# Kernel tuning notes

Measured on AMD Instinct MI355X. Metric: run time of the kernel, lower is better.

The kernel has to match this reference:

```python
import jax, jax.numpy as jnp
import numpy as np

L, B, S, D, H, FF = 6, 4, 1024, 256, 8, 128
DH = D // H
EPS = 1e-5


def _ln(x, w, b):
    m = x.mean(-1, keepdims=True)
    v = ((x - m) ** 2).mean(-1, keepdims=True)
    return (x - m) / jnp.sqrt(v + EPS) * w + b


def setup_inputs() -> dict:
    key = jax.random.key(0)
    ks = jax.random.split(key, 6)
    s = lambda k, shape: jax.random.normal(k, shape, jnp.float32) * 0.02
    return {
        "x": jax.random.normal(ks[0], (B, S, D), jnp.float32),
        "ln1_w": jnp.ones((L, D), jnp.float32),
        "ln1_b": jnp.zeros((L, D), jnp.float32),
        "wqkv": s(ks[1], (L, D, 3 * D)),   # qkv_linear, bias=False
        "wout": s(ks[2], (L, D, D)),       # out_linear, bias=False
        "ln2_w": jnp.ones((L, D), jnp.float32),
        "ln2_b": jnp.zeros((L, D), jnp.float32),
        "w1": s(ks[3], (L, D, 2 * FF)),    # Linear(d_model, 2*ff)
        "b1": jnp.zeros((L, 2 * FF), jnp.float32),
        "w2": s(ks[4], (L, FF, D)),        # Linear(ff, d_model)
        "b2": jnp.zeros((L, D), jnp.float32),
    }


def reference(x, ln1_w, ln1_b, wqkv, wout, ln2_w, ln2_b, w1, b1, w2, b2):
    attn_weights_list = []
    scale = 1.0 / jnp.sqrt(jnp.float32(DH))
    for i in range(L):
        # --- pre-norm multi-head attention ---
        xn = _ln(x, ln1_w[i], ln1_b[i])
        qkv = xn @ wqkv[i]                       # [B,S,3D]
        q, k, v = jnp.split(qkv, 3, axis=-1)
        rs = lambda t: t.reshape(B, S, H, DH).transpose(0, 2, 1, 3)  # b h s d
        q, k, v = rs(q), rs(k), rs(v)
        logits = jnp.einsum('bhid,bhjd->bhij', q, k) * scale
        aw = jax.nn.softmax(logits, axis=-1)     # [B,H,S,S] (dropout=0, eval)
        attn_weights_list.append(aw)
        o = jnp.einsum('bhij,bhjd->bhid', aw, v)
        o = o.transpose(0, 2, 1, 3).reshape(B, S, D) @ wout[i]
        x = x + o
        # --- pre-norm GEGLU FFN ---
        h = _ln(x, ln2_w[i], ln2_b[i]) @ w1[i] + b1[i]   # [B,S,2*FF]
        a, g = jnp.split(h, 2, axis=-1)
        x = x + (a * jax.nn.gelu(g, approximate=False)) @ w2[i] + b2[i]
    return x, jnp.stack(attn_weights_list)      # [B,S,D], [L,B,H,S,S]
```

## Files before the change

### kernel.cpp

```cpp
#include <hip/hip_runtime.h>
#include <hip/hip_bf16.h>

typedef __bf16 bf16x8 __attribute__((ext_vector_type(8)));
typedef __bf16 bf16x4 __attribute__((ext_vector_type(4)));
typedef __bf16 bf16x2 __attribute__((ext_vector_type(2)));
typedef float  f32x4  __attribute__((ext_vector_type(4)));

#define LAYERS 6
#define BATCH  4
#define SEQ    1024
#define DMODEL 256
#define NHEAD  8
#define DHEAD  32
#define FFDIM  128
#define ROWS   (BATCH*SEQ)
#define QKVN   (3*DMODEL)
#define QSCALE 0.2550348616f

static __device__ __forceinline__ bf16x8 ldg8(const __bf16* p) {
  return *reinterpret_cast<const bf16x8*>(p);
}
#define MFMA16(a, b, c) __builtin_amdgcn_mfma_f32_16x16x32_bf16((a), (b), (c), 0, 0, 0)

__global__ void k_prep(const float* __restrict__ wqkv, const float* __restrict__ wout,
                       const float* __restrict__ w1, const float* __restrict__ w2,
                       __bf16* __restrict__ wqkvT, __bf16* __restrict__ woutT,
                       __bf16* __restrict__ w1T, __bf16* __restrict__ w2T) {
  const int N1 = LAYERS * DMODEL * QKVN;
  const int N2 = LAYERS * DMODEL * DMODEL;
  const int N3 = LAYERS * DMODEL * 2 * FFDIM;
  const int N4 = LAYERS * FFDIM * DMODEL;
  int total = N1 + N2 + N3 + N4;
  for (int i = blockIdx.x * blockDim.x + threadIdx.x; i < total; i += gridDim.x * blockDim.x) {
    int j = i;
    if (j < N1) {
      int l = j / (DMODEL * QKVN), rc = j - l * (DMODEL * QKVN);
      int r = rc / QKVN, c = rc - r * QKVN;
      wqkvT[(size_t)l * DMODEL * QKVN + (size_t)c * DMODEL + r] = (__bf16)wqkv[j]; continue;
    } j -= N1;
    if (j < N2) {
      int l = j / (DMODEL * DMODEL), rc = j - l * (DMODEL * DMODEL);
      int r = rc / DMODEL, c = rc - r * DMODEL;
      woutT[(size_t)l * DMODEL * DMODEL + (size_t)c * DMODEL + r] = (__bf16)wout[j]; continue;
    } j -= N2;
    if (j < N3) {
      int l = j / (DMODEL * 2 * FFDIM), rc = j - l * (DMODEL * 2 * FFDIM);
      int r = rc / (2 * FFDIM), c = rc - r * (2 * FFDIM);
      w1T[(size_t)l * DMODEL * 2 * FFDIM + (size_t)c * DMODEL + r] = (__bf16)w1[j]; continue;
    } j -= N3;
    {
      int l = j / (FFDIM * DMODEL), rc = j - l * (FFDIM * DMODEL);
      int r = rc / DMODEL, c = rc - r * DMODEL;
      w2T[(size_t)l * FFDIM * DMODEL + (size_t)c * FFDIM + r] = (__bf16)w2[j];
    }
  }
}

__global__ __launch_bounds__(64) void k_ln(const float* __restrict__ x,
                                           const float* __restrict__ w,
                                           const float* __restrict__ b,
                                           __bf16* __restrict__ out) {
  int row = blockIdx.x, l = threadIdx.x;
  const float* xr = x + (size_t)row * DMODEL;
  float v[4];
  #pragma unroll
  for (int j = 0; j < 4; ++j) v[j] = xr[l + 64 * j];
  float s = v[0] + v[1] + v[2] + v[3];
  #pragma unroll
  for (int off = 32; off >= 1; off >>= 1) s += __shfl_xor(s, off);
  float mean = s * (1.0f / DMODEL);
  float sq = 0.f;
  #pragma unroll
  for (int j = 0; j < 4; ++j) { v[j] -= mean; sq += v[j] * v[j]; }
  #pragma unroll
  for (int off = 32; off >= 1; off >>= 1) sq += __shfl_xor(sq, off);
  float rstd = rsqrtf(sq * (1.0f / DMODEL) + 1e-5f);
  __bf16* orow = out + (size_t)row * DMODEL;
  #pragma unroll
  for (int j = 0; j < 4; ++j) {
    int c = l + 64 * j;
    orow[c] = (__bf16)(v[j] * rstd * w[c] + b[c]);
  }
}

__global__ __launch_bounds__(256) void k_qkv(const __bf16* __restrict__ xn,
                                             const __bf16* __restrict__ Bt,
                                             __bf16* __restrict__ qb,
                                             __bf16* __restrict__ kt,
                                             __bf16* __restrict__ vt) {
  int w = threadIdx.x >> 6, l = threadIdx.x & 63, lr = l & 15, lg = l >> 4;
  int m0 = blockIdx.x * 64 + w * 16;
  int n0 = blockIdx.y * 64;
  f32x4 acc[4] = {};
  const __bf16* ap = xn + (size_t)(m0 + lr) * DMODEL + 8 * lg;
  const __bf16* bp = Bt + (size_t)(n0 + lr) * DMODEL + 8 * lg;
  for (int kc = 0; kc < DMODEL; kc += 32) {
    bf16x8 a = ldg8(ap + kc);
    #pragma unroll
    for (int t = 0; t < 4; ++t) {
      bf16x8 b = ldg8(bp + (size_t)t * 16 * DMODEL + kc);
      acc[t] = MFMA16(a, b, acc[t]);
    }
  }
  int row = m0 + lg * 4;
  if (n0 < DMODEL) {
    #pragma unroll
    for (int t = 0; t < 4; ++t) {
      int col = n0 + t * 16 + lr;
      #pragma unroll
      for (int r = 0; r < 4; ++r)
        qb[(size_t)(row + r) * DMODEL + col] = (__bf16)(acc[t][r] * QSCALE);
    }
  } else if (n0 < 2 * DMODEL) {
    int b_ = row >> 10, s = row & (SEQ - 1);
    #pragma unroll
    for (int t = 0; t < 4; ++t) {
      int hdh = n0 - DMODEL + t * 16 + lr;
      int h = hdh >> 5, dh = hdh & 31;
      size_t base = ((size_t)(b_ * NHEAD + h) * SEQ + s) * DHEAD + dh;
      #pragma unroll
      for (int r = 0; r < 4; ++r) kt[base + (size_t)r * DHEAD] = (__bf16)acc[t][r];
    }
  } else {
    int b_ = row >> 10, s = row & (SEQ - 1);
    #pragma unroll
    for (int t = 0; t < 4; ++t) {
      int hdh = n0 - 2 * DMODEL + t * 16 + lr;
      int h = hdh >> 5, dh = hdh & 31;
      bf16x4 v4;
      #pragma unroll
      for (int r = 0; r < 4; ++r) v4[r] = (__bf16)acc[t][r];
      *reinterpret_cast<bf16x4*>(vt + ((size_t)(b_ * NHEAD + h) * DHEAD + dh) * SEQ + s) = v4;
    }
  }
}

__global__ __launch_bounds__(512, 6) void k_attn(const __bf16* __restrict__ qb,
                                                 const __bf16* __restrict__ kt,
                                                 const __bf16* __restrict__ vt,
                                                 __bf16* __restrict__ ob,
                                                 float* __restrict__ aw) {
  __shared__ __bf16 P[8][2][16][40];
  __shared__ float  Ssum[8][16];
  __shared__ float  OS[8][16][34];
  int bid = blockIdx.x;
  int swz = (bid & 7) * 256 + (bid >> 3);
  int qblk = swz & 63, h = (swz >> 6) & 7, b = swz >> 9;
  int w = threadIdx.x >> 6, l = threadIdx.x & 63, lr = l & 15, lg = l >> 4;
  int q0 = qblk * 16;
  bf16x8 qf = ldg8(qb + ((size_t)(b * SEQ) + q0 + lr) * DMODEL + h * DHEAD + 8 * lg);
  const __bf16* ktb = kt + (size_t)(b * NHEAD + h) * SEQ * DHEAD + 8 * lg;
  const __bf16* vtb = vt + (size_t)(b * NHEAD + h) * DHEAD * SEQ;
  f32x4 z = {};
  int kbeg = w * 128;

  float s4[4] = {0.f, 0.f, 0.f, 0.f};
  #pragma unroll 4
  for (int t = 0; t < 8; ++t) {
    bf16x8 kf = ldg8(ktb + (size_t)(kbeg + t * 16 + lr) * DHEAD);
    f32x4 d = MFMA16(qf, kf, z);
    #pragma unroll
    for (int r = 0; r < 4; ++r) s4[r] += exp2f(d[r]);
  }
  #pragma unroll
  for (int off = 1; off < 16; off <<= 1) {
    #pragma unroll
    for (int r = 0; r < 4; ++r) s4[r] += __shfl_xor(s4[r], off);
  }
  if (lr == 0) {
    #pragma unroll
    for (int r = 0; r < 4; ++r) Ssum[w][lg * 4 + r] = s4[r];
  }
  __syncthreads();
  float rinv[4];
  #pragma unroll
  for (int r = 0; r < 4; ++r) {
    int row = lg * 4 + r;
    float s = Ssum[0][row] + Ssum[1][row] + Ssum[2][row] + Ssum[3][row]
            + Ssum[4][row] + Ssum[5][row] + Ssum[6][row] + Ssum[7][row];
    rinv[r] = 1.0f / s;
  }

  float* awb = aw + ((size_t)(b * NHEAD + h) * SEQ) * SEQ;

#define QK_TILE(KC, BUF)                                                          \
  {                                                                               \
    _Pragma("unroll")                                                             \
    for (int half = 0; half < 2; ++half) {                                        \
      int k0 = (KC) + half * 16;                                                  \
      bf16x8 kf = ldg8(ktb + (size_t)(k0 + lr) * DHEAD);                          \
      f32x4 d = MFMA16(qf, kf, z);                                                \
      _Pragma("unroll")                                                           \
      for (int r = 0; r < 4; ++r) {                                               \
        float pv = exp2f(d[r]);                                                   \
        __builtin_nontemporal_store(pv * rinv[r],                                 \
            &awb[(size_t)(q0 + lg * 4 + r) * SEQ + k0 + lr]);                     \
        P[w][BUF][lg * 4 + r][half * 16 + lr] = (__bf16)pv;                       \
      }                                                                           \
    }                                                                             \
  }

  f32x4 accO[2] = {};
  QK_TILE(kbeg, 0)
  #pragma unroll
  for (int j = 1; j < 4; ++j) {
    int kc = kbeg + j * 32;
    bf16x8 pf  = *reinterpret_cast<const bf16x8*>(&P[w][(j - 1) & 1][lr][8 * lg]);
    bf16x8 vf0 = ldg8(vtb + (size_t)lr * SEQ + (kc - 32) + 8 * lg);
    bf16x8 vf1 = ldg8(vtb + (size_t)(16 + lr) * SEQ + (kc - 32) + 8 * lg);
    QK_TILE(kc, j & 1)
    accO[0] = MFMA16(pf, vf0, accO[0]);
    accO[1] = MFMA16(pf, vf1, accO[1]);
  }
  {
    bf16x8 pf  = *reinterpret_cast<const bf16x8*>(&P[w][1][lr][8 * lg]);
    bf16x8 vf0 = ldg8(vtb + (size_t)lr * SEQ + (kbeg + 96) + 8 * lg);
    bf16x8 vf1 = ldg8(vtb + (size_t)(16 + lr) * SEQ + (kbeg + 96) + 8 * lg);
    accO[0] = MFMA16(pf, vf0, accO[0]);
    accO[1] = MFMA16(pf, vf1, accO[1]);
  }
#undef QK_TILE

  #pragma unroll
  for (int t = 0; t < 2; ++t)
    #pragma unroll
    for (int r = 0; r < 4; ++r) OS[w][lg * 4 + r][t * 16 + lr] = accO[t][r] * rinv[r];
  __syncthreads();
  int row = threadIdx.x >> 5, col = threadIdx.x & 31;
  float o = 0.f;
  #pragma unroll
  for (int ww = 0; ww < 8; ++ww) o += OS[ww][row][col];
  ob[((size_t)(b * SEQ) + q0 + row) * DMODEL + h * DHEAD + col] = (__bf16)o;
}

template <int LAST>
__global__ __launch_bounds__(512) void k_pf(const __bf16* __restrict__ ob,
                                            const __bf16* __restrict__ woutT,
                                            const float* __restrict__ xres,
                                            const float* __restrict__ ln2w,
                                            const float* __restrict__ ln2b,
                                            const __bf16* __restrict__ w1t,
                                            const float* __restrict__ b1,
                                            const __bf16* __restrict__ w2t,
                                            const float* __restrict__ b2,
                                            float* __restrict__ x32out,
                                            const float* __restrict__ lnw_n,
                                            const float* __restrict__ lnb_n,
                                            const __bf16* __restrict__ wqkvT_n,
                                            __bf16* __restrict__ qb,
                                            __bf16* __restrict__ kt,
                                            __bf16* __restrict__ vt,
                                            float* __restrict__ xout) {
  __shared__ float  xs[16][268];
  __shared__ __bf16 XN[16][264];
  __shared__ __bf16 G[16][136];
  __shared__ __bf16 HT[16][136];
  int w = threadIdx.x >> 6, l = threadIdx.x & 63, lr = l & 15, lg = l >> 4;
  int m0 = blockIdx.x * 16;
  {
    int n0 = w * 32;
    f32x4 acc[2] = {};
    const __bf16* ap = ob + (size_t)(m0 + lr) * DMODEL + 8 * lg;
    const __bf16* bp = woutT + (size_t)(n0 + lr) * DMODEL + 8 * lg;
    for (int kc = 0; kc < DMODEL; kc += 32) {
      bf16x8 a = ldg8(ap + kc);
      #pragma unroll
      for (int t = 0; t < 2; ++t)
        acc[t] = MFMA16(a, ldg8(bp + (size_t)t * 16 * DMODEL + kc), acc[t]);
    }
    #pragma unroll
    for (int t = 0; t < 2; ++t) {
      int col = n0 + t * 16 + lr;
      #pragma unroll
      for (int r = 0; r < 4; ++r) {
        int row = lg * 4 + r;
        xs[row][col] = acc[t][r] + xres[(size_t)(m0 + row) * DMODEL + col];
      }
    }
  }
  __syncthreads();
  #pragma unroll
  for (int rr = 0; rr < 2; ++rr) {
    int row = w * 2 + rr;
    f32x4 v = *reinterpret_cast<const f32x4*>(&xs[row][4 * l]);
    float s = v[0] + v[1] + v[2] + v[3];
    #pragma unroll
    for (int off = 32; off >= 1; off >>= 1) s += __shfl_xor(s, off);
    float mean = s * (1.0f / DMODEL);
    float sq = 0.f;
    f32x4 c;
    #pragma unroll
    for (int j = 0; j < 4; ++j) { c[j] = v[j] - mean; sq += c[j] * c[j]; }
    #pragma unroll
    for (int off = 32; off >= 1; off >>= 1) sq += __shfl_xor(sq, off);
    float rstd = rsqrtf(sq * (1.0f / DMODEL) + 1e-5f);
    f32x4 lwv = *reinterpret_cast<const f32x4*>(&ln2w[4 * l]);
    f32x4 lbv = *reinterpret_cast<const f32x4*>(&ln2b[4 * l]);
    bf16x4 o4;
    #pragma unroll
    for (int j = 0; j < 4; ++j) o4[j] = (__bf16)(c[j] * rstd * lwv[j] + lbv[j]);
    *reinterpret_cast<bf16x4*>(&XN[row][4 * l]) = o4;
  }
  __syncthreads();
  int n0f = w * 32;
  f32x4 acc1[2] = {};
  {
    const __bf16* bp = w1t + (size_t)(n0f + lr) * DMODEL + 8 * lg;
    for (int kc = 0; kc < DMODEL; kc += 32) {
      bf16x8 a = *reinterpret_cast<const bf16x8*>(&XN[lr][kc + 8 * lg]);
      #pragma unroll
      for (int t = 0; t < 2; ++t)
        acc1[t] = MFMA16(a, ldg8(bp + (size_t)t * 16 * DMODEL + kc), acc1[t]);
    }
  }
  if (w >= 4) {
    #pragma unroll
    for (int t = 0; t < 2; ++t) {
      int col = n0f + t * 16 + lr;
      #pragma unroll
      for (int r = 0; r < 4; ++r) {
        float g = acc1[t][r] + b1[col];
        float ge = 0.5f * g * (1.0f + erff(g * 0.70710678118654752f));
        G[lg * 4 + r][col - 128] = (__bf16)ge;
      }
    }
  }
  __syncthreads();
  if (w < 4) {
    #pragma unroll
    for (int t = 0; t < 2; ++t) {
      int col = n0f + t * 16 + lr;
      #pragma unroll
      for (int r = 0; r < 4; ++r) {
        float a1 = acc1[t][r] + b1[col];
        HT[lg * 4 + r][col] = (__bf16)(a1 * (float)G[lg * 4 + r][col]);
      }
    }
  }
  __syncthreads();
  {
    f32x4 acc2[2] = {};
    const __bf16* bp = w2t + (size_t)(n0f + lr) * FFDIM + 8 * lg;
    for (int kc = 0; kc < FFDIM; kc += 32) {
      bf16x8 a2 = *reinterpret_cast<const bf16x8*>(&HT[lr][kc + 8 * lg]);
      #pragma unroll
      for (int t = 0; t < 2; ++t)
        acc2[t] = MFMA16(a2, ldg8(bp + (size_t)t * 16 * FFDIM + kc), acc2[t]);
    }
    #pragma unroll
    for (int t = 0; t < 2; ++t) {
      int col = n0f + t * 16 + lr;
      #pragma unroll
      for (int r = 0; r < 4; ++r) {
        int row = lg * 4 + r;
        xs[row][col] = acc2[t][r] + b2[col] + xs[row][col];
      }
    }
  }
  __syncthreads();
  #pragma unroll
  for (int rr = 0; rr < 2; ++rr) {
    int row = w * 2 + rr;
    f32x4 v = *reinterpret_cast<const f32x4*>(&xs[row][4 * l]);
    if (LAST) {
      *reinterpret_cast<f32x4*>(&xout[(size_t)(m0 + row) * DMODEL + 4 * l]) = v;
    } else {
      float s = v[0] + v[1] + v[2] + v[3];
      #pragma unroll
      for (int off = 32; off >= 1; off >>= 1) s += __shfl_xor(s, off);
      float mean = s * (1.0f / DMODEL);
      float sq = 0.f;
      f32x4 c;
      #pragma unroll
      for (int j = 0; j < 4; ++j) { c[j] = v[j] - mean; sq += c[j] * c[j]; }
      #pragma unroll
      for (int off = 32; off >= 1; off >>= 1) sq += __shfl_xor(sq, off);
      float rstd = rsqrtf(sq * (1.0f / DMODEL) + 1e-5f);
      *reinterpret_cast<f32x4*>(&x32out[(size_t)(m0 + row) * DMODEL + 4 * l]) = v;
      f32x4 lwv = *reinterpret_cast<const f32x4*>(&lnw_n[4 * l]);
      f32x4 lbv = *reinterpret_cast<const f32x4*>(&lnb_n[4 * l]);
      bf16x4 o4;
      #pragma unroll
      for (int j = 0; j < 4; ++j) o4[j] = (__bf16)(c[j] * rstd * lwv[j] + lbv[j]);
      *reinterpret_cast<bf16x4*>(&XN[row][4 * l]) = o4;
    }
  }
  if (!LAST) {
    __syncthreads();
    f32x4 acc[6] = {};
    {
      const __bf16* bp = wqkvT_n + (size_t)(w * 96 + lr) * DMODEL + 8 * lg;
      for (int kc = 0; kc < DMODEL; kc += 32) {
        bf16x8 a = *reinterpret_cast<const bf16x8*>(&XN[lr][kc + 8 * lg]);
        #pragma unroll
        for (int t = 0; t < 6; ++t)
          acc[t] = MFMA16(a, ldg8(bp + (size_t)t * 16 * DMODEL + kc), acc[t]);
      }
    }
    int row = m0 + lg * 4;
    int b_ = row >> 10, s = row & (SEQ - 1);
    #pragma unroll
    for (int t = 0; t < 6; ++t) {
      int col = w * 96 + t * 16 + lr;
      if (col < DMODEL) {
        #pragma unroll
        for (int r = 0; r < 4; ++r)
          qb[(size_t)(row + r) * DMODEL + col] = (__bf16)(acc[t][r] * QSCALE);
      } else if (col < 2 * DMODEL) {
        int hdh = col - DMODEL;
        int h = hdh >> 5, dh = hdh & 31;
        size_t base = ((size_t)(b_ * NHEAD + h) * SEQ + s) * DHEAD + dh;
        #pragma unroll
        for (int r = 0; r < 4; ++r) kt[base + (size_t)r * DHEAD] = (__bf16)acc[t][r];
      } else {
        int hdh = col - 2 * DMODEL;
        int h = hdh >> 5, dh = hdh & 31;
        bf16x4 v4;
        #pragma unroll
        for (int r = 0; r < 4; ++r) v4[r] = (__bf16)acc[t][r];
        *reinterpret_cast<bf16x4*>(vt + ((size_t)(b_ * NHEAD + h) * DHEAD + dh) * SEQ + s) = v4;
      }
    }
  }
}

static inline size_t align256(size_t x) { return (x + 255) & ~(size_t)255; }

extern "C" void kernel_launch(void* const* d_in, const int* in_sizes, int n_in,
                              void* d_out, int out_size, void* d_ws, size_t ws_size,
                              hipStream_t stream) {
  const float* x_in = (const float*)d_in[0];
  const float* ln1w = (const float*)d_in[1];
  const float* ln1b = (const float*)d_in[2];
  const float* wqkv = (const float*)d_in[3];
  const float* wout = (const float*)d_in[4];
  const float* ln2w = (const float*)d_in[5];
  const float* ln2b = (const float*)d_in[6];
  const float* w1   = (const float*)d_in[7];
  const float* b1   = (const float*)d_in[8];
  const float* w2   = (const float*)d_in[9];
  const float* b2   = (const float*)d_in[10];
  float* out = (float*)d_out;

  char* p = (char*)d_ws;
  float*  x32   = (float*)p;  p += align256((size_t)ROWS * DMODEL * 4);
  __bf16* xn    = (__bf16*)p; p += align256((size_t)ROWS * DMODEL * 2);
  __bf16* qb    = (__bf16*)p; p += align256((size_t)ROWS * DMODEL * 2);
  __bf16* kt    = (__bf16*)p; p += align256((size_t)ROWS * DMODEL * 2);
  __bf16* vt    = (__bf16*)p; p += align256((size_t)ROWS * DMODEL * 2);
  __bf16* ob    = (__bf16*)p; p += align256((size_t)ROWS * DMODEL * 2);
  __bf16* wqkvT = (__bf16*)p; p += align256((size_t)LAYERS * DMODEL * QKVN * 2);
  __bf16* woutT = (__bf16*)p; p += align256((size_t)LAYERS * DMODEL * DMODEL * 2);
  __bf16* w1T   = (__bf16*)p; p += align256((size_t)LAYERS * DMODEL * 2 * FFDIM * 2);
  __bf16* w2T   = (__bf16*)p; p += align256((size_t)LAYERS * FFDIM * DMODEL * 2);

  k_prep<<<2048, 256, 0, stream>>>(wqkv, wout, w1, w2, wqkvT, woutT, w1T, w2T);
  k_ln<<<ROWS, 64, 0, stream>>>(x_in, ln1w, ln1b, xn);
  k_qkv<<<dim3(ROWS / 64, QKVN / 64), 256, 0, stream>>>(xn, wqkvT, qb, kt, vt);

  const size_t AW_LAYER = (size_t)BATCH * NHEAD * SEQ * SEQ;
  for (int i = 0; i < LAYERS; ++i) {
    float* aw_l = out + (size_t)ROWS * DMODEL + (size_t)i * AW_LAYER;
    k_attn<<<SEQ / 16 * NHEAD * BATCH, 512, 0, stream>>>(qb, kt, vt, ob, aw_l);
    const float* xres = (i == 0) ? x_in : x32;
    if (i < LAYERS - 1) {
      k_pf<0><<<ROWS / 16, 512, 0, stream>>>(
          ob, woutT + (size_t)i * DMODEL * DMODEL, xres,
          ln2w + i * DMODEL, ln2b + i * DMODEL,
          w1T + (size_t)i * DMODEL * 2 * FFDIM, b1 + i * 2 * FFDIM,
          w2T + (size_t)i * FFDIM * DMODEL, b2 + i * DMODEL,
          x32, ln1w + (i + 1) * DMODEL, ln1b + (i + 1) * DMODEL,
          wqkvT + (size_t)(i + 1) * DMODEL * QKVN, qb, kt, vt, nullptr);
    } else {
      k_pf<1><<<ROWS / 16, 512, 0, stream>>>(
          ob, woutT + (size_t)i * DMODEL * DMODEL, xres,
          ln2w + i * DMODEL, ln2b + i * DMODEL,
          w1T + (size_t)i * DMODEL * 2 * FFDIM, b1 + i * 2 * FFDIM,
          w2T + (size_t)i * FFDIM * DMODEL, b2 + i * DMODEL,
          x32, nullptr, nullptr, nullptr, nullptr, nullptr, nullptr, out);
    }
  }
}
```

Baseline: 458.3 us.

## Fuse attention into post-attention FFN kernel with ping-pong QKV buffers

Merges the attention kernel and the out-projection/FFN/next-QKV kernel into one per-16-row block kernel. Each of the 8 waves now handles one head over the full sequence instead of splitting keys across waves, so the attention output stays in shared memory and the cross-wave reductions are no longer needed. QKV buffers are double-buffered because the next layer's Q/K/V are written while other blocks still read the current ones. This removes a launch and the global round trip of the attention output per layer. In exchange each wave runs a much longer serial key loop, grid parallelism per block drops, and larger shared memory may reduce occupancy.

```diff
diff --git a/kernel.cpp b/kernel.cpp
--- a/kernel.cpp
+++ b/kernel.cpp
@@ -3,7 +3,6 @@
 
 typedef __bf16 bf16x8 __attribute__((ext_vector_type(8)));
 typedef __bf16 bf16x4 __attribute__((ext_vector_type(4)));
-typedef __bf16 bf16x2 __attribute__((ext_vector_type(2)));
 typedef float  f32x4  __attribute__((ext_vector_type(4)));
 
 #define LAYERS 6
@@ -135,29 +134,46 @@
   }
 }
 
-__global__ __launch_bounds__(512, 6) void k_attn(const __bf16* __restrict__ qb,
-                                                 const __bf16* __restrict__ kt,
-                                                 const __bf16* __restrict__ vt,
-                                                 __bf16* __restrict__ ob,
-                                                 float* __restrict__ aw) {
+template <int LAST>
+__global__ __launch_bounds__(512) void k_mega(const __bf16* __restrict__ qb,
+                                              const __bf16* __restrict__ kt,
+                                              const __bf16* __restrict__ vt,
+                                              const __bf16* __restrict__ woutT,
+                                              const float* __restrict__ xres,
+                                              const float* __restrict__ ln2w,
+                                              const float* __restrict__ ln2b,
+                                              const __bf16* __restrict__ w1t,
+                                              const float* __restrict__ b1,
+                                              const __bf16* __restrict__ w2t,
+                                              const float* __restrict__ b2,
+                                              float* __restrict__ x32out,
+                                              const float* __restrict__ lnw_n,
+                                              const float* __restrict__ lnb_n,
+                                              const __bf16* __restrict__ wqkvT_n,
+                                              __bf16* __restrict__ qb_n,
+                                              __bf16* __restrict__ kt_n,
+                                              __bf16* __restrict__ vt_n,
+                                              float* __restrict__ aw,
+                                              float* __restrict__ xout) {
   __shared__ __bf16 P[8][2][16][40];
-  __shared__ float  Ssum[8][16];
-  __shared__ float  OS[8][16][34];
-  int bid = blockIdx.x;
-  int swz = (bid & 7) * 256 + (bid >> 3);
-  int qblk = swz & 63, h = (swz >> 6) & 7, b = swz >> 9;
+  __shared__ __bf16 OB[16][264];
+  __shared__ float  xs[16][268];
+  __shared__ __bf16 XN[16][264];
+  __shared__ __bf16 G[16][136];
+  __shared__ __bf16 HT[16][136];
   int w = threadIdx.x >> 6, l = threadIdx.x & 63, lr = l & 15, lg = l >> 4;
-  int q0 = qblk * 16;
-  bf16x8 qf = ldg8(qb + ((size_t)(b * SEQ) + q0 + lr) * DMODEL + h * DHEAD + 8 * lg);
-  const __bf16* ktb = kt + (size_t)(b * NHEAD + h) * SEQ * DHEAD + 8 * lg;
-  const __bf16* vtb = vt + (size_t)(b * NHEAD + h) * DHEAD * SEQ;
+  int m0 = blockIdx.x * 16;
+  int b = m0 >> 10, q0 = m0 & (SEQ - 1);
+
+  bf16x8 qf = ldg8(qb + (size_t)(m0 + lr) * DMODEL + w * DHEAD + 8 * lg);
+  const __bf16* ktb = kt + (size_t)(b * NHEAD + w) * SEQ * DHEAD + 8 * lg;
+  const __bf16* vtb = vt + (size_t)(b * NHEAD + w) * DHEAD * SEQ;
   f32x4 z = {};
-  int kbeg = w * 128;
 
   float s4[4] = {0.f, 0.f, 0.f, 0.f};
   #pragma unroll 4
-  for (int t = 0; t < 8; ++t) {
-    bf16x8 kf = ldg8(ktb + (size_t)(kbeg + t * 16 + lr) * DHEAD);
+  for (int t = 0; t < SEQ / 16; ++t) {
+    bf16x8 kf = ldg8(ktb + (size_t)(t * 16 + lr) * DHEAD);
     f32x4 d = MFMA16(qf, kf, z);
     #pragma unroll
     for (int r = 0; r < 4; ++r) s4[r] += exp2f(d[r]);
@@ -167,21 +183,11 @@
     #pragma unroll
     for (int r = 0; r < 4; ++r) s4[r] += __shfl_xor(s4[r], off);
   }
-  if (lr == 0) {
-    #pragma unroll
-    for (int r = 0; r < 4; ++r) Ssum[w][lg * 4 + r] = s4[r];
-  }
-  __syncthreads();
   float rinv[4];
   #pragma unroll
-  for (int r = 0; r < 4; ++r) {
-    int row = lg * 4 + r;
-    float s = Ssum[0][row] + Ssum[1][row] + Ssum[2][row] + Ssum[3][row]
-            + Ssum[4][row] + Ssum[5][row] + Ssum[6][row] + Ssum[7][row];
-    rinv[r] = 1.0f / s;
-  }
-
-  float* awb = aw + ((size_t)(b * NHEAD + h) * SEQ) * SEQ;
+  for (int r = 0; r < 4; ++r) rinv[r] = 1.0f / s4[r];
+
+  float* awb = aw + ((size_t)(b * NHEAD + w) * SEQ) * SEQ;
 
 #define QK_TILE(KC, BUF)                                                          \
   {                                                                               \
@@ -201,10 +207,10 @@
   }
 
   f32x4 accO[2] = {};
-  QK_TILE(kbeg, 0)
-  #pragma unroll
-  for (int j = 1; j < 4; ++j) {
-    int kc = kbeg + j * 32;
+  QK_TILE(0, 0)
+  #pragma unroll 2
+  for (int j = 1; j < SEQ / 32; ++j) {
+    int kc = j * 32;
     bf16x8 pf  = *reinterpret_cast<const bf16x8*>(&P[w][(j - 1) & 1][lr][8 * lg]);
     bf16x8 vf0 = ldg8(vtb + (size_t)lr * SEQ + (kc - 32) + 8 * lg);
     bf16x8 vf1 = ldg8(vtb + (size_t)(16 + lr) * SEQ + (kc - 32) + 8 * lg);
@@ -214,8 +220,8 @@
   }
   {
     bf16x8 pf  = *reinterpret_cast<const bf16x8*>(&P[w][1][lr][8 * lg]);
-    bf16x8 vf0 = ldg8(vtb + (size_t)lr * SEQ + (kbeg + 96) + 8 * lg);
-    bf16x8 vf1 = ldg8(vtb + (size_t)(16 + lr) * SEQ + (kbeg + 96) + 8 * lg);
+    bf16x8 vf0 = ldg8(vtb + (size_t)lr * SEQ + (SEQ - 32) + 8 * lg);
+    bf16x8 vf1 = ldg8(vtb + (size_t)(16 + lr) * SEQ + (SEQ - 32) + 8 * lg);
     accO[0] = MFMA16(pf, vf0, accO[0]);
     accO[1] = MFMA16(pf, vf1, accO[1]);
   }
@@ -224,46 +230,16 @@
   #pragma unroll
   for (int t = 0; t < 2; ++t)
     #pragma unroll
-    for (int r = 0; r < 4; ++r) OS[w][lg * 4 + r][t * 16 + lr] = accO[t][r] * rinv[r];
-  __syncthreads();
-  int row = threadIdx.x >> 5, col = threadIdx.x & 31;
-  float o = 0.f;
-  #pragma unroll
-  for (int ww = 0; ww < 8; ++ww) o += OS[ww][row][col];
-  ob[((size_t)(b * SEQ) + q0 + row) * DMODEL + h * DHEAD + col] = (__bf16)o;
-}
-
-template <int LAST>
-__global__ __launch_bounds__(512) void k_pf(const __bf16* __restrict__ ob,
-                                            const __bf16* __restrict__ woutT,
-                                            const float* __restrict__ xres,
-                                            const float* __restrict__ ln2w,
-                                            const float* __restrict__ ln2b,
-                                            const __bf16* __restrict__ w1t,
-                                            const float* __restrict__ b1,
-                                            const __bf16* __restrict__ w2t,
-                                            const float* __restrict__ b2,
-                                            float* __restrict__ x32out,
-                                            const float* __restrict__ lnw_n,
-                                            const float* __restrict__ lnb_n,
-                                            const __bf16* __restrict__ wqkvT_n,
-                                            __bf16* __restrict__ qb,
-                                            __bf16* __restrict__ kt,
-                                            __bf16* __restrict__ vt,
-                                            float* __restrict__ xout) {
-  __shared__ float  xs[16][268];
-  __shared__ __bf16 XN[16][264];
-  __shared__ __bf16 G[16][136];
-  __shared__ __bf16 HT[16][136];
-  int w = threadIdx.x >> 6, l = threadIdx.x & 63, lr = l & 15, lg = l >> 4;
-  int m0 = blockIdx.x * 16;
+    for (int r = 0; r < 4; ++r)
+      OB[lg * 4 + r][w * DHEAD + t * 16 + lr] = (__bf16)(accO[t][r] * rinv[r]);
+  __syncthreads();
+
   {
     int n0 = w * 32;
     f32x4 acc[2] = {};
-    const __bf16* ap = ob + (size_t)(m0 + lr) * DMODEL + 8 * lg;
     const __bf16* bp = woutT + (size_t)(n0 + lr) * DMODEL + 8 * lg;
     for (int kc = 0; kc < DMODEL; kc += 32) {
-      bf16x8 a = ldg8(ap + kc);
+      bf16x8 a = *reinterpret_cast<const bf16x8*>(&OB[lr][kc + 8 * lg]);
       #pragma unroll
       for (int t = 0; t < 2; ++t)
         acc[t] = MFMA16(a, ldg8(bp + (size_t)t * 16 * DMODEL + kc), acc[t]);
@@ -405,20 +381,20 @@
       if (col < DMODEL) {
         #pragma unroll
         for (int r = 0; r < 4; ++r)
-          qb[(size_t)(row + r) * DMODEL + col] = (__bf16)(acc[t][r] * QSCALE);
+          qb_n[(size_t)(row + r) * DMODEL + col] = (__bf16)(acc[t][r] * QSCALE);
       } else if (col < 2 * DMODEL) {
         int hdh = col - DMODEL;
         int h = hdh >> 5, dh = hdh & 31;
         size_t base = ((size_t)(b_ * NHEAD + h) * SEQ + s) * DHEAD + dh;
         #pragma unroll
-        for (int r = 0; r < 4; ++r) kt[base + (size_t)r * DHEAD] = (__bf16)acc[t][r];
+        for (int r = 0; r < 4; ++r) kt_n[base + (size_t)r * DHEAD] = (__bf16)acc[t][r];
       } else {
         int hdh = col - 2 * DMODEL;
         int h = hdh >> 5, dh = hdh & 31;
         bf16x4 v4;
         #pragma unroll
         for (int r = 0; r < 4; ++r) v4[r] = (__bf16)acc[t][r];
-        *reinterpret_cast<bf16x4*>(vt + ((size_t)(b_ * NHEAD + h) * DHEAD + dh) * SEQ + s) = v4;
+        *reinterpret_cast<bf16x4*>(vt_n + ((size_t)(b_ * NHEAD + h) * DHEAD + dh) * SEQ + s) = v4;
       }
     }
   }
@@ -445,10 +421,12 @@
   char* p = (char*)d_ws;
   float*  x32   = (float*)p;  p += align256((size_t)ROWS * DMODEL * 4);
   __bf16* xn    = (__bf16*)p; p += align256((size_t)ROWS * DMODEL * 2);
-  __bf16* qb    = (__bf16*)p; p += align256((size_t)ROWS * DMODEL * 2);
-  __bf16* kt    = (__bf16*)p; p += align256((size_t)ROWS * DMODEL * 2);
-  __bf16* vt    = (__bf16*)p; p += align256((size_t)ROWS * DMODEL * 2);
-  __bf16* ob    = (__bf16*)p; p += align256((size_t)ROWS * DMODEL * 2);
+  __bf16* qbA   = (__bf16*)p; p += align256((size_t)ROWS * DMODEL * 2);
+  __bf16* ktA   = (__bf16*)p; p += align256((size_t)ROWS * DMODEL * 2);
+  __bf16* vtA   = (__bf16*)p; p += align256((size_t)ROWS * DMODEL * 2);
+  __bf16* qbB   = (__bf16*)p; p += align256((size_t)ROWS * DMODEL * 2);
+  __bf16* ktB   = (__bf16*)p; p += align256((size_t)ROWS * DMODEL * 2);
+  __bf16* vtB   = (__bf16*)p; p += align256((size_t)ROWS * DMODEL * 2);
   __bf16* wqkvT = (__bf16*)p; p += align256((size_t)LAYERS * DMODEL * QKVN * 2);
   __bf16* woutT = (__bf16*)p; p += align256((size_t)LAYERS * DMODEL * DMODEL * 2);
   __bf16* w1T   = (__bf16*)p; p += align256((size_t)LAYERS * DMODEL * 2 * FFDIM * 2);
@@ -456,28 +434,35 @@
 
   k_prep<<<2048, 256, 0, stream>>>(wqkv, wout, w1, w2, wqkvT, woutT, w1T, w2T);
   k_ln<<<ROWS, 64, 0, stream>>>(x_in, ln1w, ln1b, xn);
-  k_qkv<<<dim3(ROWS / 64, QKVN / 64), 256, 0, stream>>>(xn, wqkvT, qb, kt, vt);
+  k_qkv<<<dim3(ROWS / 64, QKVN / 64), 256, 0, stream>>>(xn, wqkvT, qbA, ktA, vtA);
 
   const size_t AW_LAYER = (size_t)BATCH * NHEAD * SEQ * SEQ;
   for (int i = 0; i < LAYERS; ++i) {
     float* aw_l = out + (size_t)ROWS * DMODEL + (size_t)i * AW_LAYER;
-    k_attn<<<SEQ / 16 * NHEAD * BATCH, 512, 0, stream>>>(qb, kt, vt, ob, aw_l);
     const float* xres = (i == 0) ? x_in : x32;
+    __bf16* qb_c = (i & 1) ? qbB : qbA;
+    __bf16* kt_c = (i & 1) ? ktB : ktA;
+    __bf16* vt_c = (i & 1) ? vtB : vtA;
+    __bf16* qb_n = (i & 1) ? qbA : qbB;
+    __bf16* kt_n = (i & 1) ? ktA : ktB;
+    __bf16* vt_n = (i & 1) ? vtA : vtB;
     if (i < LAYERS - 1) {
-      k_pf<0><<<ROWS / 16, 512, 0, stream>>>(
-          ob, woutT + (size_t)i * DMODEL * DMODEL, xres,
+      k_mega<0><<<ROWS / 16, 512, 0, stream>>>(
+          qb_c, kt_c, vt_c, woutT + (size_t)i * DMODEL * DMODEL, xres,
           ln2w + i * DMODEL, ln2b + i * DMODEL,
           w1T + (size_t)i * DMODEL * 2 * FFDIM, b1 + i * 2 * FFDIM,
           w2T + (size_t)i * FFDIM * DMODEL, b2 + i * DMODEL,
           x32, ln1w + (i + 1) * DMODEL, ln1b + (i + 1) * DMODEL,
-          wqkvT + (size_t)(i + 1) * DMODEL * QKVN, qb, kt, vt, nullptr);
+          wqkvT + (size_t)(i + 1) * DMODEL * QKVN, qb_n, kt_n, vt_n,
+          aw_l, nullptr);
     } else {
-      k_pf<1><<<ROWS / 16, 512, 0, stream>>>(
-          ob, woutT + (size_t)i * DMODEL * DMODEL, xres,
+      k_mega<1><<<ROWS / 16, 512, 0, stream>>>(
+          qb_c, kt_c, vt_c, woutT + (size_t)i * DMODEL * DMODEL, xres,
           ln2w + i * DMODEL, ln2b + i * DMODEL,
           w1T + (size_t)i * DMODEL * 2 * FFDIM, b1 + i * 2 * FFDIM,
           w2T + (size_t)i * FFDIM * DMODEL, b2 + i * DMODEL,
-          x32, nullptr, nullptr, nullptr, nullptr, nullptr, nullptr, out);
-    }
-  }
-}
+          x32, nullptr, nullptr, nullptr, nullptr, nullptr, nullptr,
+          aw_l, out);
+    }
+  }
+}
```

Result: slower. 531.1 us (+15.9%).

## Move attention-weight output writes into post-attention kernel with double-buffered QKV

Applied to the files above, without the earlier changes.

The attention kernel no longer runs a separate pass to compute softmax denominators and no longer writes the full attention-weight matrix. It accumulates row sums during its single QK pass and writes per-row reciprocal sums to a small buffer. The following fused projection/FFN kernel then recomputes QK^T for its 16 rows across all heads, normalizes the values, and streams them out with coalesced vector stores staged through shared memory. Q/K/V buffers are double-buffered so the next layer's QKV can be written while the current ones are still being read. The cost is redundant QK MFMA work and a larger workspace, in exchange for removing the duplicated QK pass and moving the large output write to a better-shaped store pattern.

```diff
diff --git a/kernel.cpp b/kernel.cpp
--- a/kernel.cpp
+++ b/kernel.cpp
@@ -3,7 +3,6 @@
 
 typedef __bf16 bf16x8 __attribute__((ext_vector_type(8)));
 typedef __bf16 bf16x4 __attribute__((ext_vector_type(4)));
-typedef __bf16 bf16x2 __attribute__((ext_vector_type(2)));
 typedef float  f32x4  __attribute__((ext_vector_type(4)));
 
 #define LAYERS 6
@@ -139,7 +138,7 @@
                                                  const __bf16* __restrict__ kt,
                                                  const __bf16* __restrict__ vt,
                                                  __bf16* __restrict__ ob,
-                                                 float* __restrict__ aw) {
+                                                 float* __restrict__ rb) {
   __shared__ __bf16 P[8][2][16][40];
   __shared__ float  Ssum[8][16];
   __shared__ float  OS[8][16][34];
@@ -155,33 +154,6 @@
   int kbeg = w * 128;
 
   float s4[4] = {0.f, 0.f, 0.f, 0.f};
-  #pragma unroll 4
-  for (int t = 0; t < 8; ++t) {
-    bf16x8 kf = ldg8(ktb + (size_t)(kbeg + t * 16 + lr) * DHEAD);
-    f32x4 d = MFMA16(qf, kf, z);
-    #pragma unroll
-    for (int r = 0; r < 4; ++r) s4[r] += exp2f(d[r]);
-  }
-  #pragma unroll
-  for (int off = 1; off < 16; off <<= 1) {
-    #pragma unroll
-    for (int r = 0; r < 4; ++r) s4[r] += __shfl_xor(s4[r], off);
-  }
-  if (lr == 0) {
-    #pragma unroll
-    for (int r = 0; r < 4; ++r) Ssum[w][lg * 4 + r] = s4[r];
-  }
-  __syncthreads();
-  float rinv[4];
-  #pragma unroll
-  for (int r = 0; r < 4; ++r) {
-    int row = lg * 4 + r;
-    float s = Ssum[0][row] + Ssum[1][row] + Ssum[2][row] + Ssum[3][row]
-            + Ssum[4][row] + Ssum[5][row] + Ssum[6][row] + Ssum[7][row];
-    rinv[r] = 1.0f / s;
-  }
-
-  float* awb = aw + ((size_t)(b * NHEAD + h) * SEQ) * SEQ;
 
 #define QK_TILE(KC, BUF)                                                          \
   {                                                                               \
@@ -193,8 +165,7 @@
       _Pragma("unroll")                                                           \
       for (int r = 0; r < 4; ++r) {                                               \
         float pv = exp2f(d[r]);                                                   \
-        __builtin_nontemporal_store(pv * rinv[r],                                 \
-            &awb[(size_t)(q0 + lg * 4 + r) * SEQ + k0 + lr]);                     \
+        s4[r] += pv;                                                              \
         P[w][BUF][lg * 4 + r][half * 16 + lr] = (__bf16)pv;                       \
       }                                                                           \
     }                                                                             \
@@ -222,6 +193,31 @@
 #undef QK_TILE
 
   #pragma unroll
+  for (int off = 1; off < 16; off <<= 1) {
+    #pragma unroll
+    for (int r = 0; r < 4; ++r) s4[r] += __shfl_xor(s4[r], off);
+  }
+  if (lr == 0) {
+    #pragma unroll
+    for (int r = 0; r < 4; ++r) Ssum[w][lg * 4 + r] = s4[r];
+  }
+  __syncthreads();
+  float rinv[4];
+  #pragma unroll
+  for (int r = 0; r < 4; ++r) {
+    int row = lg * 4 + r;
+    float s = Ssum[0][row] + Ssum[1][row] + Ssum[2][row] + Ssum[3][row]
+            + Ssum[4][row] + Ssum[5][row] + Ssum[6][row] + Ssum[7][row];
+    rinv[r] = 1.0f / s;
+  }
+  if (w == 0 && l < 16) {
+    float s = 0.f;
+    #pragma unroll
+    for (int ww = 0; ww < 8; ++ww) s += Ssum[ww][l];
+    rb[((size_t)(b * SEQ) + q0 + l) * NHEAD + h] = 1.0f / s;
+  }
+
+  #pragma unroll
   for (int t = 0; t < 2; ++t)
     #pragma unroll
     for (int r = 0; r < 4; ++r) OS[w][lg * 4 + r][t * 16 + lr] = accO[t][r] * rinv[r];
@@ -235,6 +231,10 @@
 
 template <int LAST>
 __global__ __launch_bounds__(512) void k_pf(const __bf16* __restrict__ ob,
+                                            const __bf16* __restrict__ qbr,
+                                            const __bf16* __restrict__ ktr,
+                                            const float* __restrict__ rb,
+                                            float* __restrict__ aw,
                                             const __bf16* __restrict__ woutT,
                                             const float* __restrict__ xres,
                                             const float* __restrict__ ln2w,
@@ -247,9 +247,9 @@
                                             const float* __restrict__ lnw_n,
                                             const float* __restrict__ lnb_n,
                                             const __bf16* __restrict__ wqkvT_n,
-                                            __bf16* __restrict__ qb,
-                                            __bf16* __restrict__ kt,
-                                            __bf16* __restrict__ vt,
+                                            __bf16* __restrict__ qb_n,
+                                            __bf16* __restrict__ kt_n,
+                                            __bf16* __restrict__ vt_n,
                                             float* __restrict__ xout) {
   __shared__ float  xs[16][268];
   __shared__ __bf16 XN[16][264];
@@ -257,6 +257,36 @@
   __shared__ __bf16 HT[16][136];
   int w = threadIdx.x >> 6, l = threadIdx.x & 63, lr = l & 15, lg = l >> 4;
   int m0 = blockIdx.x * 16;
+  int b = m0 >> 10, q0 = m0 & (SEQ - 1);
+  f32x4 z = {};
+
+  {
+    float (*ST)[32] = reinterpret_cast<float(*)[32]>(&xs[0][0]) + w * 16;
+    bf16x8 qf = ldg8(qbr + (size_t)(m0 + lr) * DMODEL + w * DHEAD + 8 * lg);
+    const __bf16* ktb = ktr + (size_t)(b * NHEAD + w) * SEQ * DHEAD + 8 * lg;
+    float rv[4];
+    #pragma unroll
+    for (int r = 0; r < 4; ++r) rv[r] = rb[(size_t)(m0 + lg * 4 + r) * NHEAD + w];
+    float* awr = aw + ((size_t)(b * NHEAD + w) * SEQ + q0) * SEQ;
+    #pragma unroll 2
+    for (int t0 = 0; t0 < SEQ / 16; ++t0) {
+      bf16x8 kf = ldg8(ktb + (size_t)(t0 * 16 + lr) * DHEAD);
+      f32x4 d = MFMA16(qf, kf, z);
+      #pragma unroll
+      for (int r = 0; r < 4; ++r)
+        ST[lg * 4 + r][(t0 & 1) * 16 + lr] = exp2f(d[r]) * rv[r];
+      if (t0 & 1) {
+        int frow = l >> 3, fcol = (l & 7) * 4;
+        f32x4 v0 = *reinterpret_cast<const f32x4*>(&ST[frow][fcol]);
+        f32x4 v1 = *reinterpret_cast<const f32x4*>(&ST[frow + 8][fcol]);
+        int kc = (t0 - 1) * 16;
+        *reinterpret_cast<f32x4*>(&awr[(size_t)frow * SEQ + kc + fcol]) = v0;
+        *reinterpret_cast<f32x4*>(&awr[(size_t)(frow + 8) * SEQ + kc + fcol]) = v1;
+      }
+    }
+  }
+  __syncthreads();
+
   {
     int n0 = w * 32;
     f32x4 acc[2] = {};
@@ -268,6 +298,7 @@
       for (int t = 0; t < 2; ++t)
         acc[t] = MFMA16(a, ldg8(bp + (size_t)t * 16 * DMODEL + kc), acc[t]);
     }
+    __syncthreads();
     #pragma unroll
     for (int t = 0; t < 2; ++t) {
       int col = n0 + t * 16 + lr;
@@ -405,20 +436,20 @@
       if (col < DMODEL) {
         #pragma unroll
         for (int r = 0; r < 4; ++r)
-          qb[(size_t)(row + r) * DMODEL + col] = (__bf16)(acc[t][r] * QSCALE);
+          qb_n[(size_t)(row + r) * DMODEL + col] = (__bf16)(acc[t][r] * QSCALE);
       } else if (col < 2 * DMODEL) {
         int hdh = col - DMODEL;
         int h = hdh >> 5, dh = hdh & 31;
         size_t base = ((size_t)(b_ * NHEAD + h) * SEQ + s) * DHEAD + dh;
         #pragma unroll
-        for (int r = 0; r < 4; ++r) kt[base + (size_t)r * DHEAD] = (__bf16)acc[t][r];
+        for (int r = 0; r < 4; ++r) kt_n[base + (size_t)r * DHEAD] = (__bf16)acc[t][r];
       } else {
         int hdh = col - 2 * DMODEL;
         int h = hdh >> 5, dh = hdh & 31;
         bf16x4 v4;
         #pragma unroll
         for (int r = 0; r < 4; ++r) v4[r] = (__bf16)acc[t][r];
-        *reinterpret_cast<bf16x4*>(vt + ((size_t)(b_ * NHEAD + h) * DHEAD + dh) * SEQ + s) = v4;
+        *reinterpret_cast<bf16x4*>(vt_n + ((size_t)(b_ * NHEAD + h) * DHEAD + dh) * SEQ + s) = v4;
       }
     }
   }
@@ -445,10 +476,14 @@
   char* p = (char*)d_ws;
   float*  x32   = (float*)p;  p += align256((size_t)ROWS * DMODEL * 4);
   __bf16* xn    = (__bf16*)p; p += align256((size_t)ROWS * DMODEL * 2);
-  __bf16* qb    = (__bf16*)p; p += align256((size_t)ROWS * DMODEL * 2);
-  __bf16* kt    = (__bf16*)p; p += align256((size_t)ROWS * DMODEL * 2);
-  __bf16* vt    = (__bf16*)p; p += align256((size_t)ROWS * DMODEL * 2);
+  __bf16* qbA   = (__bf16*)p; p += align256((size_t)ROWS * DMODEL * 2);
+  __bf16* ktA   = (__bf16*)p; p += align256((size_t)ROWS * DMODEL * 2);
+  __bf16* vtA   = (__bf16*)p; p += align256((size_t)ROWS * DMODEL * 2);
+  __bf16* qbB   = (__bf16*)p; p += align256((size_t)ROWS * DMODEL * 2);
+  __bf16* ktB   = (__bf16*)p; p += align256((size_t)ROWS * DMODEL * 2);
+  __bf16* vtB   = (__bf16*)p; p += align256((size_t)ROWS * DMODEL * 2);
   __bf16* ob    = (__bf16*)p; p += align256((size_t)ROWS * DMODEL * 2);
+  float*  rb    = (float*)p;  p += align256((size_t)ROWS * NHEAD * 4);
   __bf16* wqkvT = (__bf16*)p; p += align256((size_t)LAYERS * DMODEL * QKVN * 2);
   __bf16* woutT = (__bf16*)p; p += align256((size_t)LAYERS * DMODEL * DMODEL * 2);
   __bf16* w1T   = (__bf16*)p; p += align256((size_t)LAYERS * DMODEL * 2 * FFDIM * 2);
@@ -456,24 +491,32 @@
 
   k_prep<<<2048, 256, 0, stream>>>(wqkv, wout, w1, w2, wqkvT, woutT, w1T, w2T);
   k_ln<<<ROWS, 64, 0, stream>>>(x_in, ln1w, ln1b, xn);
-  k_qkv<<<dim3(ROWS / 64, QKVN / 64), 256, 0, stream>>>(xn, wqkvT, qb, kt, vt);
+  k_qkv<<<dim3(ROWS / 64, QKVN / 64), 256, 0, stream>>>(xn, wqkvT, qbA, ktA, vtA);
 
   const size_t AW_LAYER = (size_t)BATCH * NHEAD * SEQ * SEQ;
   for (int i = 0; i < LAYERS; ++i) {
     float* aw_l = out + (size_t)ROWS * DMODEL + (size_t)i * AW_LAYER;
-    k_attn<<<SEQ / 16 * NHEAD * BATCH, 512, 0, stream>>>(qb, kt, vt, ob, aw_l);
     const float* xres = (i == 0) ? x_in : x32;
+    __bf16* qb_c = (i & 1) ? qbB : qbA;
+    __bf16* kt_c = (i & 1) ? ktB : ktA;
+    __bf16* vt_c = (i & 1) ? vtB : vtA;
+    __bf16* qb_n = (i & 1) ? qbA : qbB;
+    __bf16* kt_n = (i & 1) ? ktA : ktB;
+    __bf16* vt_n = (i & 1) ? vtA : vtB;
+    k_attn<<<SEQ / 16 * NHEAD * BATCH, 512, 0, stream>>>(qb_c, kt_c, vt_c, ob, rb);
     if (i < LAYERS - 1) {
       k_pf<0><<<ROWS / 16, 512, 0, stream>>>(
-          ob, woutT + (size_t)i * DMODEL * DMODEL, xres,
+          ob, qb_c, kt_c, rb, aw_l,
+          woutT + (size_t)i * DMODEL * DMODEL, xres,
           ln2w + i * DMODEL, ln2b + i * DMODEL,
           w1T + (size_t)i * DMODEL * 2 * FFDIM, b1 + i * 2 * FFDIM,
           w2T + (size_t)i * FFDIM * DMODEL, b2 + i * DMODEL,
           x32, ln1w + (i + 1) * DMODEL, ln1b + (i + 1) * DMODEL,
-          wqkvT + (size_t)(i + 1) * DMODEL * QKVN, qb, kt, vt, nullptr);
+          wqkvT + (size_t)(i + 1) * DMODEL * QKVN, qb_n, kt_n, vt_n, nullptr);
     } else {
       k_pf<1><<<ROWS / 16, 512, 0, stream>>>(
-          ob, woutT + (size_t)i * DMODEL * DMODEL, xres,
+          ob, qb_c, kt_c, rb, aw_l,
+          woutT + (size_t)i * DMODEL * DMODEL, xres,
           ln2w + i * DMODEL, ln2b + i * DMODEL,
           w1T + (size_t)i * DMODEL * 2 * FFDIM, b1 + i * 2 * FFDIM,
           w2T + (size_t)i * FFDIM * DMODEL, b2 + i * DMODEL,
```

Result: slower. 548.5 us (+19.7%).
